# Optimization experiments

Measured on AMD Instinct MI355X. Metric: run time of the kernel, lower is better.

## Reference

```python
import jax, jax.numpy as jnp
import numpy as np

B, V, J, H, W = 32, 2, 17, 128, 128
TEMP = 0.05   # SoftArgmax2D softmax_temp
EPS = 1e-12


def _soft_argmax(hm):
    # hm: (B*V, J, H, W) -> homogeneous coords (B*V, 3, J), per-joint max value
    bv, j, h, w = hm.shape
    p = jax.nn.softmax(hm.reshape(bv, j, h * w) / TEMP, axis=-1).reshape(bv, j, h, w)
    xs = jnp.arange(w, dtype=hm.dtype)
    ys = jnp.arange(h, dtype=hm.dtype)
    x = jnp.einsum('bjhw,w->bj', p, xs)
    y = jnp.einsum('bjhw,h->bj', p, ys)
    coords = jnp.stack([x, y, jnp.ones_like(x)], axis=1)  # (bv, 3, j)
    maxv = hm.max(axis=(-2, -1))
    return coords, maxv


def _skew(t):
    # t: (..., 3) -> skew-symmetric (..., 3, 3), matches -t_mat^T + t_mat in source
    tx, ty, tz = t[..., 0], t[..., 1], t[..., 2]
    z = jnp.zeros_like(tx)
    return jnp.stack([jnp.stack([z, -tz, ty], -1),
                      jnp.stack([tz, z, -tx], -1),
                      jnp.stack([-ty, tx, z], -1)], -2)


def _forward(origin_hms, AP_K, AP_T, LAT_K, LAT_T):
    K = jnp.stack([AP_K, LAT_K], axis=1)              # (B,V,3,3)
    T = jnp.stack([AP_T, LAT_T], axis=1)              # (B,V,4,4)
    R = T[:, :, :3, :3]
    t_std = T[:, :, :3, 3]                            # (B,V,3) standard_cam_T

    # fundamental matrices for all ordered pairs: cam1 = view j, cam2 = view i
    r = jnp.einsum('bimk,bjnk->bijmn', R, R)          # R_i @ R_j^T
    t = t_std[:, :, None, :] - jnp.einsum('bijmn,bjn->bijm', r, t_std)
    M = jnp.einsum('bijmn,bijnk->bijmk', _skew(t), r)
    invK = jnp.linalg.inv(K)
    # F = invK_i^T @ [t]x @ r @ invK_j
    F = jnp.einsum('bipm,bijpq,bjql->bijml', invK, M, invK)  # (B,V,V,3,3)

    coords, maxv = _soft_argmax(origin_hms)           # (B*V,3,J), (B*V,J)
    inv_aff = jnp.diag(jnp.asarray([4.0, 4.0, 1.0], dtype=origin_hms.dtype))  # inverse of 0.25 scale
    img = jnp.einsum('mn,bvnj->bvmj', inv_aff, coords.reshape(B, V, 3, J))
    confi = maxv.reshape(B, V, J)

    # epipolar distances, fully vectorized over (b, i, j) pairs
    l = jnp.einsum('bijmn,bjnk->bijmk', F, img)       # epipolar lines in view i from joints of view j
    cv = img[:, :, None]                              # (B,V,1,3,J)
    num = jnp.sum(cv * l, axis=3) ** 2                # (B,V,V,J)
    lp = jnp.einsum('bijnm,bink->bijmk', F, img)      # F^T @ cv_joints
    div = l[..., 0, :] ** 2 + l[..., 1, :] ** 2 + lp[..., 0, :] ** 2 + lp[..., 1, :] ** 2
    dist_full = jnp.sqrt(num / (div + EPS))           # (B,V,V,J)

    others = np.asarray([[j for j in range(V) if j != i] for i in range(V)])  # (V,V-1)
    ii = np.repeat(np.arange(V)[:, None], V - 1, axis=1)
    distances = dist_full[:, ii, others]              # (B,V,V-1,J)

    # stand-in for ViewWeightNet: confidence minus mean epipolar error, softmax over views
    score = confi - distances.mean(axis=2)            # (B,V,J)
    vw = jax.nn.softmax(score, axis=1)                # (B,V,J)

    mv = jnp.where(maxv > 0.01, maxv, 1e6).reshape(B * V, J, 1, 1)
    hms_norm = origin_hms / mv
    hm4 = hms_norm.reshape(B, V, J, H, W)

    # cat order: self heatmap first, then other views (matches get_warp_weight / cat_hm layout)
    order = np.asarray([[i] + [j for j in range(V) if j != i] for i in range(V)])  # (V,V)
    cat_hm = hm4[:, order]                            # (B,V,V,J,H,W); identity-warp stand-in for CamFusionModule
    ww = vw[:, order]                                 # (B,V,V,J) warp weights
    fused_hm = jnp.sum(ww[..., None, None] * cat_hm, axis=2).reshape(B * V, J, H, W)

    coords2, _ = _soft_argmax(fused_hm)
    img2 = jnp.einsum('mn,bvnj->bvmj', inv_aff, coords2.reshape(B, V, 3, J))
    return img2[:, :, :2, :], fused_hm


def setup_inputs() -> dict:
    key = jax.random.key(0)
    k1, k2, k3, k4, k5 = jax.random.split(key, 5)
    hms = jax.random.uniform(k1, (B * V, J, H, W), dtype=jnp.float32)

    def make_K(k):
        f = 1000.0 + jax.random.normal(k, (B,)) * 10.0
        Km = jnp.zeros((B, 3, 3), dtype=jnp.float32)
        Km = Km.at[:, 0, 0].set(f).at[:, 1, 1].set(f)
        Km = Km.at[:, 0, 2].set(256.0).at[:, 1, 2].set(256.0).at[:, 2, 2].set(1.0)
        return Km

    def make_T(k):
        A = jax.random.normal(k, (B, 3, 3))
        Q, _ = jnp.linalg.qr(A)
        Q = Q * jnp.linalg.det(Q)[:, None, None]  # force det = +1 (proper rotation)
        t = jax.random.normal(jax.random.fold_in(k, 1), (B, 3, 1)) * 0.1 + jnp.asarray([0.0, 0.0, 5.0]).reshape(3, 1)
        bottom = jnp.tile(jnp.asarray([[[0.0, 0.0, 0.0, 1.0]]]), (B, 1, 1))
        return jnp.concatenate([jnp.concatenate([Q, t], axis=2), bottom], axis=1).astype(jnp.float32)

    return {"origin_hms": hms, "AP_K": make_K(k2), "AP_T": make_T(k3),
            "LAT_K": make_K(k4), "LAT_T": make_T(k5)}


def reference(origin_hms, AP_K, AP_T, LAT_K, LAT_T):
    return _forward(origin_hms, AP_K, AP_T, LAT_K, LAT_T)
```

## Files before the change

kernel.cpp:

```cpp
#include <hip/hip_runtime.h>
#include <math.h>

#define NB 32
#define NV 2
#define NJ 17
#define NH 128
#define NW 128
#define MAPN (NH * NW)
#define MAPN4 (MAPN / 4)
#define NMAPS (NB * NV * NJ)
#define NBJ (NB * NJ)
#define OUT0N (NB * NV * 2 * NJ)
#define INV_TEMP 20.0f
#define EPS_D 1e-12f

#define S_CHUNKS 4
#define S_F4 (MAPN4 / S_CHUNKS)
#define F_CHUNKS 8
#define F_F4 (MAPN4 / F_CHUNKS)

#define WS_STATS_B (NMAPS * S_CHUNKS * 16)
#define WS_W_B (NBJ * 2 * 4)
#define WS_F_B (NBJ * F_CHUNKS * 16)
#define WS_NEEDED (WS_STATS_B + WS_W_B + WS_F_B)

typedef float vfloat4 __attribute__((ext_vector_type(4)));

__device__ __forceinline__ float waveMax(float v) {
#pragma unroll
    for (int off = 32; off > 0; off >>= 1)
        v = fmaxf(v, __shfl_xor(v, off, 64));
    return v;
}
__device__ __forceinline__ float waveSum(float v) {
#pragma unroll
    for (int off = 32; off > 0; off >>= 1)
        v += __shfl_xor(v, off, 64);
    return v;
}

__device__ __forceinline__ void inv3(const float K[3][3], float o[3][3]) {
    const float a = K[0][0], b = K[0][1], c = K[0][2];
    const float d = K[1][0], e = K[1][1], f = K[1][2];
    const float g = K[2][0], h = K[2][1], i = K[2][2];
    const float A =  (e * i - f * h);
    const float Bv = -(d * i - f * g);
    const float C =  (d * h - e * g);
    const float det = a * A + b * Bv + c * C;
    const float id = 1.0f / det;
    o[0][0] = A * id;  o[0][1] = -(b * i - c * h) * id;  o[0][2] = (b * f - c * e) * id;
    o[1][0] = Bv * id; o[1][1] = (a * i - c * g) * id;   o[1][2] = -(a * f - c * d) * id;
    o[2][0] = C * id;  o[2][1] = -(a * h - b * g) * id;  o[2][2] = (a * e - b * d) * id;
}

__global__ __launch_bounds__(256, 4) void k_stats(const float* __restrict__ hms,
                                                  float* __restrict__ ws) {
    const int blk = blockIdx.x;
    const int mi = blk >> 2, c = blk & 3;
    const int tid = threadIdx.x, wid = tid >> 6, lane = tid & 63;
    const float4* A = (const float4*)hms + (size_t)mi * MAPN4 + (size_t)c * S_F4;

    float mx = -1e30f, s = 0.f, sx = 0.f, sy = 0.f;
#pragma unroll
    for (int k = 0; k < 4; ++k) {
        const int i4 = tid + k * 256;
        const float4 v = A[i4];
        const int e0 = (c * S_F4 + i4) * 4;
        const float hh = (float)(e0 >> 7);
        const float ww = (float)(e0 & 127);
        mx = fmaxf(mx, fmaxf(fmaxf(v.x, v.y), fmaxf(v.z, v.w)));
        const float ea = __expf((v.x - 1.0f) * INV_TEMP);
        const float eb = __expf((v.y - 1.0f) * INV_TEMP);
        const float ec = __expf((v.z - 1.0f) * INV_TEMP);
        const float ed = __expf((v.w - 1.0f) * INV_TEMP);
        const float se = (ea + eb) + (ec + ed);
        s += se; sy += se * hh;
        sx += ea * ww + eb * (ww + 1.f) + ec * (ww + 2.f) + ed * (ww + 3.f);
    }

    mx = waveMax(mx); s = waveSum(s); sx = waveSum(sx); sy = waveSum(sy);
    __shared__ float red[4][4];
    if (lane == 0) { red[0][wid] = mx; red[1][wid] = s; red[2][wid] = sx; red[3][wid] = sy; }
    __syncthreads();
    if (tid == 0) {
        float M = red[0][0], S = red[1][0], SX = red[2][0], SY = red[3][0];
#pragma unroll
        for (int w = 1; w < 4; ++w) {
            M = fmaxf(M, red[0][w]); S += red[1][w]; SX += red[2][w]; SY += red[3][w];
        }
        ((float4*)ws)[blk] = make_float4(M, S, SX, SY);
    }
}

__global__ void k_weights(const float* __restrict__ ws_stats,
                          const float* __restrict__ APK, const float* __restrict__ APT,
                          const float* __restrict__ LATK, const float* __restrict__ LATT,
                          float* __restrict__ wsw) {
    const int bj = blockIdx.x * 64 + threadIdx.x;
    if (bj >= NBJ) return;
    const int b = bj / NJ, j = bj % NJ;

    float conf[2], img[2][3];
    const float4* st = (const float4*)ws_stats;
#pragma unroll
    for (int v = 0; v < 2; ++v) {
        const int mi = (b * 2 + v) * NJ + j;
        float M = -1e30f, S = 0.f, SX = 0.f, SY = 0.f;
#pragma unroll
        for (int c = 0; c < S_CHUNKS; ++c) {
            const float4 p = st[mi * S_CHUNKS + c];
            M = fmaxf(M, p.x); S += p.y; SX += p.z; SY += p.w;
        }
        conf[v] = M;
        img[v][0] = 4.0f * (SX / S);
        img[v][1] = 4.0f * (SY / S);
        img[v][2] = 1.0f;
    }

    float F[2][3][3];
    {
        float Km[2][3][3], R[2][3][3], tr[2][3], iK[2][3][3];
        for (int r = 0; r < 3; ++r)
            for (int cc = 0; cc < 3; ++cc) {
                Km[0][r][cc] = APK[b * 9 + r * 3 + cc];
                Km[1][r][cc] = LATK[b * 9 + r * 3 + cc];
                R[0][r][cc] = APT[b * 16 + r * 4 + cc];
                R[1][r][cc] = LATT[b * 16 + r * 4 + cc];
            }
        for (int r = 0; r < 3; ++r) {
            tr[0][r] = APT[b * 16 + r * 4 + 3];
            tr[1][r] = LATT[b * 16 + r * 4 + 3];
        }
        inv3(Km[0], iK[0]);
        inv3(Km[1], iK[1]);

        for (int i = 0; i < 2; ++i) {
            const int jj = 1 - i;
            float r[3][3];
            for (int m = 0; m < 3; ++m)
                for (int n = 0; n < 3; ++n)
                    r[m][n] = R[i][m][0] * R[jj][n][0] + R[i][m][1] * R[jj][n][1] + R[i][m][2] * R[jj][n][2];
            float tv[3];
            for (int m = 0; m < 3; ++m)
                tv[m] = tr[i][m] - (r[m][0] * tr[jj][0] + r[m][1] * tr[jj][1] + r[m][2] * tr[jj][2]);
            const float S[3][3] = {{0.f, -tv[2], tv[1]}, {tv[2], 0.f, -tv[0]}, {-tv[1], tv[0], 0.f}};
            float M[3][3];
            for (int m = 0; m < 3; ++m)
                for (int n = 0; n < 3; ++n)
                    M[m][n] = S[m][0] * r[0][n] + S[m][1] * r[1][n] + S[m][2] * r[2][n];
            float tmp[3][3];
            for (int p = 0; p < 3; ++p)
                for (int l = 0; l < 3; ++l)
                    tmp[p][l] = M[p][0] * iK[jj][0][l] + M[p][1] * iK[jj][1][l] + M[p][2] * iK[jj][2][l];
            for (int m = 0; m < 3; ++m)
                for (int l = 0; l < 3; ++l)
                    F[i][m][l] = iK[i][0][m] * tmp[0][l] + iK[i][1][m] * tmp[1][l] + iK[i][2][m] * tmp[2][l];
        }
    }

    float score[2];
#pragma unroll
    for (int i = 0; i < 2; ++i) {
        const int jj = 1 - i;
        const float l0 = F[i][0][0] * img[jj][0] + F[i][0][1] * img[jj][1] + F[i][0][2] * img[jj][2];
        const float l1 = F[i][1][0] * img[jj][0] + F[i][1][1] * img[jj][1] + F[i][1][2] * img[jj][2];
        const float l2 = F[i][2][0] * img[jj][0] + F[i][2][1] * img[jj][1] + F[i][2][2] * img[jj][2];
        const float sdot = img[i][0] * l0 + img[i][1] * l1 + img[i][2] * l2;
        const float num = sdot * sdot;
        const float lp0 = F[i][0][0] * img[i][0] + F[i][1][0] * img[i][1] + F[i][2][0] * img[i][2];
        const float lp1 = F[i][0][1] * img[i][0] + F[i][1][1] * img[i][1] + F[i][2][1] * img[i][2];
        const float dv = l0 * l0 + l1 * l1 + lp0 * lp0 + lp1 * lp1;
        score[i] = conf[i] - sqrtf(num / (dv + EPS_D));
    }
    const float mS = fmaxf(score[0], score[1]);
    const float e0w = __expf(score[0] - mS), e1w = __expf(score[1] - mS);
    const float inv = 1.0f / (e0w + e1w);
    const float mv0 = conf[0] > 0.01f ? conf[0] : 1e6f;
    const float mv1 = conf[1] > 0.01f ? conf[1] : 1e6f;
    wsw[bj * 2 + 0] = (e0w * inv) / mv0;
    wsw[bj * 2 + 1] = (e1w * inv) / mv1;
}

__global__ __launch_bounds__(256, 4) void k_fuse(const float* __restrict__ hms,
                                                 const float* __restrict__ wsw,
                                                 float* __restrict__ out,
                                                 float* __restrict__ wsf) {
    const int blk = blockIdx.x;
    const int bj = blk >> 3, c = blk & 7;
    const int b = bj / NJ, j = bj % NJ;
    const int tid = threadIdx.x, wid = tid >> 6, lane = tid & 63;

    const float w0 = wsw[bj * 2 + 0];
    const float w1 = wsw[bj * 2 + 1];

    const size_t m0 = ((size_t)(b * 2 + 0) * NJ + j) * MAPN4;
    const size_t m1 = ((size_t)(b * 2 + 1) * NJ + j) * MAPN4;
    const float4* A  = (const float4*)hms + m0 + (size_t)c * F_F4;
    const float4* Bp = (const float4*)hms + m1 + (size_t)c * F_F4;
    float* outhm = out + OUT0N;
    vfloat4* O0 = reinterpret_cast<vfloat4*>(outhm) + m0 + (size_t)c * F_F4;
    vfloat4* O1 = reinterpret_cast<vfloat4*>(outhm) + m1 + (size_t)c * F_F4;

    float s = 0.f, sx = 0.f, sy = 0.f;
#pragma unroll
    for (int k = 0; k < 2; ++k) {
        const int i4 = tid + k * 256;
        const float4 a = A[i4];
        const float4 cc = Bp[i4];
        vfloat4 f;
        f.x = w0 * a.x + w1 * cc.x;
        f.y = w0 * a.y + w1 * cc.y;
        f.z = w0 * a.z + w1 * cc.z;
        f.w = w0 * a.w + w1 * cc.w;
        __builtin_nontemporal_store(f, &O0[i4]);
        __builtin_nontemporal_store(f, &O1[i4]);
        const int e0 = (c * F_F4 + i4) * 4;
        const float hh = (float)(e0 >> 7);
        const float ww = (float)(e0 & 127);
        const float ea = __expf((f.x - 1.0f) * INV_TEMP);
        const float eb = __expf((f.y - 1.0f) * INV_TEMP);
        const float ec = __expf((f.z - 1.0f) * INV_TEMP);
        const float ed = __expf((f.w - 1.0f) * INV_TEMP);
        const float se = (ea + eb) + (ec + ed);
        s += se; sy += se * hh;
        sx += ea * ww + eb * (ww + 1.f) + ec * (ww + 2.f) + ed * (ww + 3.f);
    }

    s = waveSum(s); sx = waveSum(sx); sy = waveSum(sy);
    __shared__ float red[3][4];
    if (lane == 0) { red[0][wid] = s; red[1][wid] = sx; red[2][wid] = sy; }
    __syncthreads();
    if (tid == 0) {
        float S = red[0][0], SX = red[1][0], SY = red[2][0];
#pragma unroll
        for (int w = 1; w < 4; ++w) { S += red[0][w]; SX += red[1][w]; SY += red[2][w]; }
        ((float4*)wsf)[blk] = make_float4(S, SX, SY, 0.f);
    }
}

__global__ void k_out(const float* __restrict__ wsf, float* __restrict__ out) {
    const int bj = blockIdx.x * 64 + threadIdx.x;
    if (bj >= NBJ) return;
    const int b = bj / NJ, j = bj % NJ;
    const float4* p = (const float4*)wsf + bj * F_CHUNKS;
    float S = 0.f, SX = 0.f, SY = 0.f;
#pragma unroll
    for (int c = 0; c < F_CHUNKS; ++c) {
        const float4 q = p[c];
        S += q.x; SX += q.y; SY += q.z;
    }
    const float x4 = 4.0f * (SX / S);
    const float y4 = 4.0f * (SY / S);
    out[((b * 2 + 0) * 2 + 0) * NJ + j] = x4;
    out[((b * 2 + 0) * 2 + 1) * NJ + j] = y4;
    out[((b * 2 + 1) * 2 + 0) * NJ + j] = x4;
    out[((b * 2 + 1) * 2 + 1) * NJ + j] = y4;
}

__global__ __launch_bounds__(512, 2) void k_one(const float* __restrict__ hms,
                                                const float* __restrict__ APK,
                                                const float* __restrict__ APT,
                                                const float* __restrict__ LATK,
                                                const float* __restrict__ LATT,
                                                float* __restrict__ out) {
    const int blk = blockIdx.x;
    const int b = blk / NJ, j = blk % NJ;
    const int tid = threadIdx.x;
    const int wid = tid >> 6, lane = tid & 63;

    float F[2][3][3];
    {
        float Km[2][3][3], R[2][3][3], tr[2][3], iK[2][3][3];
        for (int r = 0; r < 3; ++r)
            for (int c = 0; c < 3; ++c) {
                Km[0][r][c] = APK[b * 9 + r * 3 + c];
                Km[1][r][c] = LATK[b * 9 + r * 3 + c];
                R[0][r][c] = APT[b * 16 + r * 4 + c];
                R[1][r][c] = LATT[b * 16 + r * 4 + c];
            }
        for (int r = 0; r < 3; ++r) {
            tr[0][r] = APT[b * 16 + r * 4 + 3];
            tr[1][r] = LATT[b * 16 + r * 4 + 3];
        }
        inv3(Km[0], iK[0]);
        inv3(Km[1], iK[1]);

        for (int i = 0; i < 2; ++i) {
            const int jj = 1 - i;
            float r[3][3];
            for (int m = 0; m < 3; ++m)
                for (int n = 0; n < 3; ++n)
                    r[m][n] = R[i][m][0] * R[jj][n][0] + R[i][m][1] * R[jj][n][1] + R[i][m][2] * R[jj][n][2];
            float tv[3];
            for (int m = 0; m < 3; ++m)
                tv[m] = tr[i][m] - (r[m][0] * tr[jj][0] + r[m][1] * tr[jj][1] + r[m][2] * tr[jj][2]);
            const float S[3][3] = {{0.f, -tv[2], tv[1]}, {tv[2], 0.f, -tv[0]}, {-tv[1], tv[0], 0.f}};
            float M[3][3];
            for (int m = 0; m < 3; ++m)
                for (int n = 0; n < 3; ++n)
                    M[m][n] = S[m][0] * r[0][n] + S[m][1] * r[1][n] + S[m][2] * r[2][n];
            float tmp[3][3];
            for (int p = 0; p < 3; ++p)
                for (int l = 0; l < 3; ++l)
                    tmp[p][l] = M[p][0] * iK[jj][0][l] + M[p][1] * iK[jj][1][l] + M[p][2] * iK[jj][2][l];
            for (int m = 0; m < 3; ++m)
                for (int l = 0; l < 3; ++l)
                    F[i][m][l] = iK[i][0][m] * tmp[0][l] + iK[i][1][m] * tmp[1][l] + iK[i][2][m] * tmp[2][l];
        }
    }

    const int idx0 = (b * 2 + 0) * NJ + j;
    const int idx1 = (b * 2 + 1) * NJ + j;
    const size_t m0 = (size_t)idx0 * MAPN4;
    const size_t m1 = (size_t)idx1 * MAPN4;
    const float4* A  = (const float4*)hms + m0;
    const float4* Bp = (const float4*)hms + m1;

    float4 va[8];
    float mx0 = -1e30f, s0 = 0.f, sx0 = 0.f, sy0 = 0.f;
    float mx1 = -1e30f, s1 = 0.f, sx1 = 0.f, sy1 = 0.f;
#pragma unroll
    for (int u = 0; u < 8; ++u) {
        const int i4 = tid + u * 512;
        const float4 v = A[i4];
        const float4 w = Bp[i4];
        va[u] = v;
        const int e0 = i4 * 4;
        const float hh = (float)(e0 >> 7);
        const float ww = (float)(e0 & 127);
        {
            mx0 = fmaxf(mx0, fmaxf(fmaxf(v.x, v.y), fmaxf(v.z, v.w)));
            const float ea = __expf((v.x - 1.0f) * INV_TEMP);
            const float eb = __expf((v.y - 1.0f) * INV_TEMP);
            const float ec = __expf((v.z - 1.0f) * INV_TEMP);
            const float ed = __expf((v.w - 1.0f) * INV_TEMP);
            const float se = (ea + eb) + (ec + ed);
            s0 += se; sy0 += se * hh;
            sx0 += ea * ww + eb * (ww + 1.f) + ec * (ww + 2.f) + ed * (ww + 3.f);
        }
        {
            mx1 = fmaxf(mx1, fmaxf(fmaxf(w.x, w.y), fmaxf(w.z, w.w)));
            const float ea = __expf((w.x - 1.0f) * INV_TEMP);
            const float eb = __expf((w.y - 1.0f) * INV_TEMP);
            const float ec = __expf((w.z - 1.0f) * INV_TEMP);
            const float ed = __expf((w.w - 1.0f) * INV_TEMP);
            const float se = (ea + eb) + (ec + ed);
            s1 += se; sy1 += se * hh;
            sx1 += ea * ww + eb * (ww + 1.f) + ec * (ww + 2.f) + ed * (ww + 3.f);
        }
    }

    __shared__ float red[8][8];
    mx0 = waveMax(mx0); mx1 = waveMax(mx1);
    s0 = waveSum(s0); sx0 = waveSum(sx0); sy0 = waveSum(sy0);
    s1 = waveSum(s1); sx1 = waveSum(sx1); sy1 = waveSum(sy1);
    if (lane == 0) {
        red[0][wid] = mx0; red[1][wid] = s0; red[2][wid] = sx0; red[3][wid] = sy0;
        red[4][wid] = mx1; red[5][wid] = s1; red[6][wid] = sx1; red[7][wid] = sy1;
    }
    __syncthreads();
    float M0 = red[0][0], S0 = red[1][0], SX0 = red[2][0], SY0 = red[3][0];
    float M1 = red[4][0], S1 = red[5][0], SX1 = red[6][0], SY1 = red[7][0];
#pragma unroll
    for (int w = 1; w < 8; ++w) {
        M0 = fmaxf(M0, red[0][w]); S0 += red[1][w]; SX0 += red[2][w]; SY0 += red[3][w];
        M1 = fmaxf(M1, red[4][w]); S1 += red[5][w]; SX1 += red[6][w]; SY1 += red[7][w];
    }

    float w0, w1;
    {
        const float conf[2] = {M0, M1};
        float img[2][3];
        img[0][0] = 4.0f * (SX0 / S0); img[0][1] = 4.0f * (SY0 / S0); img[0][2] = 1.0f;
        img[1][0] = 4.0f * (SX1 / S1); img[1][1] = 4.0f * (SY1 / S1); img[1][2] = 1.0f;

        float score[2];
        for (int i = 0; i < 2; ++i) {
            const int jj = 1 - i;
            const float l0 = F[i][0][0] * img[jj][0] + F[i][0][1] * img[jj][1] + F[i][0][2] * img[jj][2];
            const float l1 = F[i][1][0] * img[jj][0] + F[i][1][1] * img[jj][1] + F[i][1][2] * img[jj][2];
            const float l2 = F[i][2][0] * img[jj][0] + F[i][2][1] * img[jj][1] + F[i][2][2] * img[jj][2];
            const float sdot = img[i][0] * l0 + img[i][1] * l1 + img[i][2] * l2;
            const float num = sdot * sdot;
            const float lp0 = F[i][0][0] * img[i][0] + F[i][1][0] * img[i][1] + F[i][2][0] * img[i][2];
            const float lp1 = F[i][0][1] * img[i][0] + F[i][1][1] * img[i][1] + F[i][2][1] * img[i][2];
            const float dv = l0 * l0 + l1 * l1 + lp0 * lp0 + lp1 * lp1;
            score[i] = conf[i] - sqrtf(num / (dv + EPS_D));
        }
        const float mS = fmaxf(score[0], score[1]);
        const float e0w = __expf(score[0] - mS), e1w = __expf(score[1] - mS);
        const float inv = 1.0f / (e0w + e1w);
        const float mv0 = conf[0] > 0.01f ? conf[0] : 1e6f;
        const float mv1 = conf[1] > 0.01f ? conf[1] : 1e6f;
        w0 = (e0w * inv) / mv0;
        w1 = (e1w * inv) / mv1;
    }

    float* outhm = out + OUT0N;
    vfloat4* O0 = reinterpret_cast<vfloat4*>(outhm) + m0;
    vfloat4* O1 = reinterpret_cast<vfloat4*>(outhm) + m1;

    float s = 0.f, sx = 0.f, sy = 0.f;
#pragma unroll
    for (int u = 0; u < 8; ++u) {
        const int i4 = tid + u * 512;
        const float4 a = va[u];
        const float4 c = Bp[i4];
        vfloat4 f;
        f.x = w0 * a.x + w1 * c.x;
        f.y = w0 * a.y + w1 * c.y;
        f.z = w0 * a.z + w1 * c.z;
        f.w = w0 * a.w + w1 * c.w;
        __builtin_nontemporal_store(f, &O0[i4]);
        __builtin_nontemporal_store(f, &O1[i4]);
        const int e0 = i4 * 4;
        const float hh = (float)(e0 >> 7);
        const float ww = (float)(e0 & 127);
        const float ea = __expf((f.x - 1.0f) * INV_TEMP);
        const float eb = __expf((f.y - 1.0f) * INV_TEMP);
        const float ec = __expf((f.z - 1.0f) * INV_TEMP);
        const float ed = __expf((f.w - 1.0f) * INV_TEMP);
        const float se = (ea + eb) + (ec + ed);
        s += se; sy += se * hh;
        sx += ea * ww + eb * (ww + 1.f) + ec * (ww + 2.f) + ed * (ww + 3.f);
    }

    __syncthreads();
    s = waveSum(s); sx = waveSum(sx); sy = waveSum(sy);
    if (lane == 0) { red[0][wid] = s; red[1][wid] = sx; red[2][wid] = sy; }
    __syncthreads();
    if (tid == 0) {
        float S = red[0][0], SX = red[1][0], SY = red[2][0];
#pragma unroll
        for (int w = 1; w < 8; ++w) { S += red[0][w]; SX += red[1][w]; SY += red[2][w]; }
        const float x4 = 4.0f * (SX / S);
        const float y4 = 4.0f * (SY / S);
        out[((b * 2 + 0) * 2 + 0) * NJ + j] = x4;
        out[((b * 2 + 0) * 2 + 1) * NJ + j] = y4;
        out[((b * 2 + 1) * 2 + 0) * NJ + j] = x4;
        out[((b * 2 + 1) * 2 + 1) * NJ + j] = y4;
    }
}

extern "C" void kernel_launch(void* const* d_in, const int* in_sizes, int n_in,
                              void* d_out, int out_size, void* d_ws, size_t ws_size,
                              hipStream_t stream) {
    const float* hms  = (const float*)d_in[0];
    const float* APK  = (const float*)d_in[1];
    const float* APT  = (const float*)d_in[2];
    const float* LATK = (const float*)d_in[3];
    const float* LATT = (const float*)d_in[4];
    float* out = (float*)d_out;

    if (d_ws != nullptr && ws_size >= (size_t)WS_NEEDED) {
        float* ws_stats = (float*)d_ws;
        float* ws_w = ws_stats + NMAPS * S_CHUNKS * 4;
        float* ws_f = ws_w + NBJ * 2;
        k_stats<<<NMAPS * S_CHUNKS, 256, 0, stream>>>(hms, ws_stats);
        k_weights<<<(NBJ + 63) / 64, 64, 0, stream>>>(ws_stats, APK, APT, LATK, LATT, ws_w);
        k_fuse<<<NBJ * F_CHUNKS, 256, 0, stream>>>(hms, ws_w, out, ws_f);
        k_out<<<(NBJ + 63) / 64, 64, 0, stream>>>(ws_f, out);
    } else {
        k_one<<<NBJ, 512, 0, stream>>>(hms, APK, APT, LATK, LATT, out);
    }
}
```

Baseline: 141.9 us.

## Fold weight and output kernels into stats and fuse kernels

Reduces the four-kernel pipeline to two. The fundamental matrices are computed once per batch inside the stats kernel, and the per-joint view weights are recomputed inside each fuse block. The final coordinate reduction is handled by the last-arriving block through an atomic counter with threadfences. In the fuse kernel the heatmap loads are issued before the weight computation so their latency overlaps it, and k_stats launch bounds rise to 8 blocks per CU. This removes two small-kernel launches and their serialization gaps, at the cost of redundant per-block weight arithmetic and atomic synchronization.

```diff
diff --git a/kernel.cpp b/kernel.cpp
--- a/kernel.cpp
+++ b/kernel.cpp
@@ -19,10 +19,11 @@
 #define F_CHUNKS 8
 #define F_F4 (MAPN4 / F_CHUNKS)
 
-#define WS_STATS_B (NMAPS * S_CHUNKS * 16)
-#define WS_W_B (NBJ * 2 * 4)
-#define WS_F_B (NBJ * F_CHUNKS * 16)
-#define WS_NEEDED (WS_STATS_B + WS_W_B + WS_F_B)
+#define WS_STATS_F (NMAPS * S_CHUNKS * 4)
+#define WS_F_F (32 * 20)
+#define WS_CNT_F (NBJ)
+#define WS_FP_F (NBJ * F_CHUNKS * 4)
+#define WS_NEEDED ((WS_STATS_F + WS_F_F + WS_CNT_F + WS_FP_F) * 4)
 
 typedef float vfloat4 __attribute__((ext_vector_type(4)));
 
@@ -53,11 +54,71 @@
     o[2][0] = C * id;  o[2][1] = -(a * h - b * g) * id;  o[2][2] = (a * e - b * d) * id;
 }
 
-__global__ __launch_bounds__(256, 4) void k_stats(const float* __restrict__ hms,
-                                                  float* __restrict__ ws) {
+__device__ void computeF(int b, const float* APK, const float* APT,
+                         const float* LATK, const float* LATT, float F[2][3][3]) {
+    float Km[2][3][3], R[2][3][3], tr[2][3], iK[2][3][3];
+    for (int r = 0; r < 3; ++r)
+        for (int cc = 0; cc < 3; ++cc) {
+            Km[0][r][cc] = APK[b * 9 + r * 3 + cc];
+            Km[1][r][cc] = LATK[b * 9 + r * 3 + cc];
+            R[0][r][cc] = APT[b * 16 + r * 4 + cc];
+            R[1][r][cc] = LATT[b * 16 + r * 4 + cc];
+        }
+    for (int r = 0; r < 3; ++r) {
+        tr[0][r] = APT[b * 16 + r * 4 + 3];
+        tr[1][r] = LATT[b * 16 + r * 4 + 3];
+    }
+    inv3(Km[0], iK[0]);
+    inv3(Km[1], iK[1]);
+
+    for (int i = 0; i < 2; ++i) {
+        const int jj = 1 - i;
+        float r[3][3];
+        for (int m = 0; m < 3; ++m)
+            for (int n = 0; n < 3; ++n)
+                r[m][n] = R[i][m][0] * R[jj][n][0] + R[i][m][1] * R[jj][n][1] + R[i][m][2] * R[jj][n][2];
+        float tv[3];
+        for (int m = 0; m < 3; ++m)
+            tv[m] = tr[i][m] - (r[m][0] * tr[jj][0] + r[m][1] * tr[jj][1] + r[m][2] * tr[jj][2]);
+        const float S[3][3] = {{0.f, -tv[2], tv[1]}, {tv[2], 0.f, -tv[0]}, {-tv[1], tv[0], 0.f}};
+        float M[3][3];
+        for (int m = 0; m < 3; ++m)
+            for (int n = 0; n < 3; ++n)
+                M[m][n] = S[m][0] * r[0][n] + S[m][1] * r[1][n] + S[m][2] * r[2][n];
+        float tmp[3][3];
+        for (int p = 0; p < 3; ++p)
+            for (int l = 0; l < 3; ++l)
+                tmp[p][l] = M[p][0] * iK[jj][0][l] + M[p][1] * iK[jj][1][l] + M[p][2] * iK[jj][2][l];
+        for (int m = 0; m < 3; ++m)
+            for (int l = 0; l < 3; ++l)
+                F[i][m][l] = iK[i][0][m] * tmp[0][l] + iK[i][1][m] * tmp[1][l] + iK[i][2][m] * tmp[2][l];
+    }
+}
+
+__global__ __launch_bounds__(256, 8) void k_stats(const float* __restrict__ hms,
+                                                  const float* __restrict__ APK,
+                                                  const float* __restrict__ APT,
+                                                  const float* __restrict__ LATK,
+                                                  const float* __restrict__ LATT,
+                                                  float* __restrict__ ws_stats,
+                                                  float* __restrict__ wsF,
+                                                  unsigned int* __restrict__ cnt) {
     const int blk = blockIdx.x;
     const int mi = blk >> 2, c = blk & 3;
     const int tid = threadIdx.x, wid = tid >> 6, lane = tid & 63;
+
+    if (tid == 64 && blk < NBJ) cnt[blk] = 0u;
+    if (tid == 128 && blk < NB) {
+        float F[2][3][3];
+        computeF(blk, APK, APT, LATK, LATT, F);
+        float* d = wsF + blk * 20;
+#pragma unroll
+        for (int i = 0; i < 2; ++i)
+            for (int m = 0; m < 3; ++m)
+                for (int l = 0; l < 3; ++l)
+                    d[i * 9 + m * 3 + l] = F[i][m][l];
+    }
+
     const float4* A = (const float4*)hms + (size_t)mi * MAPN4 + (size_t)c * S_F4;
 
     float mx = -1e30f, s = 0.f, sx = 0.f, sy = 0.f;
@@ -88,115 +149,85 @@
         for (int w = 1; w < 4; ++w) {
             M = fmaxf(M, red[0][w]); S += red[1][w]; SX += red[2][w]; SY += red[3][w];
         }
-        ((float4*)ws)[blk] = make_float4(M, S, SX, SY);
-    }
-}
-
-__global__ void k_weights(const float* __restrict__ ws_stats,
-                          const float* __restrict__ APK, const float* __restrict__ APT,
-                          const float* __restrict__ LATK, const float* __restrict__ LATT,
-                          float* __restrict__ wsw) {
-    const int bj = blockIdx.x * 64 + threadIdx.x;
-    if (bj >= NBJ) return;
-    const int b = bj / NJ, j = bj % NJ;
-
-    float conf[2], img[2][3];
-    const float4* st = (const float4*)ws_stats;
-#pragma unroll
-    for (int v = 0; v < 2; ++v) {
-        const int mi = (b * 2 + v) * NJ + j;
-        float M = -1e30f, S = 0.f, SX = 0.f, SY = 0.f;
-#pragma unroll
-        for (int c = 0; c < S_CHUNKS; ++c) {
-            const float4 p = st[mi * S_CHUNKS + c];
-            M = fmaxf(M, p.x); S += p.y; SX += p.z; SY += p.w;
-        }
-        conf[v] = M;
-        img[v][0] = 4.0f * (SX / S);
-        img[v][1] = 4.0f * (SY / S);
-        img[v][2] = 1.0f;
-    }
-
-    float F[2][3][3];
-    {
-        float Km[2][3][3], R[2][3][3], tr[2][3], iK[2][3][3];
-        for (int r = 0; r < 3; ++r)
-            for (int cc = 0; cc < 3; ++cc) {
-                Km[0][r][cc] = APK[b * 9 + r * 3 + cc];
-                Km[1][r][cc] = LATK[b * 9 + r * 3 + cc];
-                R[0][r][cc] = APT[b * 16 + r * 4 + cc];
-                R[1][r][cc] = LATT[b * 16 + r * 4 + cc];
-            }
-        for (int r = 0; r < 3; ++r) {
-            tr[0][r] = APT[b * 16 + r * 4 + 3];
-            tr[1][r] = LATT[b * 16 + r * 4 + 3];
-        }
-        inv3(Km[0], iK[0]);
-        inv3(Km[1], iK[1]);
-
-        for (int i = 0; i < 2; ++i) {
-            const int jj = 1 - i;
-            float r[3][3];
-            for (int m = 0; m < 3; ++m)
-                for (int n = 0; n < 3; ++n)
-                    r[m][n] = R[i][m][0] * R[jj][n][0] + R[i][m][1] * R[jj][n][1] + R[i][m][2] * R[jj][n][2];
-            float tv[3];
-            for (int m = 0; m < 3; ++m)
-                tv[m] = tr[i][m] - (r[m][0] * tr[jj][0] + r[m][1] * tr[jj][1] + r[m][2] * tr[jj][2]);
-            const float S[3][3] = {{0.f, -tv[2], tv[1]}, {tv[2], 0.f, -tv[0]}, {-tv[1], tv[0], 0.f}};
-            float M[3][3];
-            for (int m = 0; m < 3; ++m)
-                for (int n = 0; n < 3; ++n)
-                    M[m][n] = S[m][0] * r[0][n] + S[m][1] * r[1][n] + S[m][2] * r[2][n];
-            float tmp[3][3];
-            for (int p = 0; p < 3; ++p)
-                for (int l = 0; l < 3; ++l)
-                    tmp[p][l] = M[p][0] * iK[jj][0][l] + M[p][1] * iK[jj][1][l] + M[p][2] * iK[jj][2][l];
-            for (int m = 0; m < 3; ++m)
-                for (int l = 0; l < 3; ++l)
-                    F[i][m][l] = iK[i][0][m] * tmp[0][l] + iK[i][1][m] * tmp[1][l] + iK[i][2][m] * tmp[2][l];
-        }
-    }
-
-    float score[2];
-#pragma unroll
-    for (int i = 0; i < 2; ++i) {
-        const int jj = 1 - i;
-        const float l0 = F[i][0][0] * img[jj][0] + F[i][0][1] * img[jj][1] + F[i][0][2] * img[jj][2];
-        const float l1 = F[i][1][0] * img[jj][0] + F[i][1][1] * img[jj][1] + F[i][1][2] * img[jj][2];
-        const float l2 = F[i][2][0] * img[jj][0] + F[i][2][1] * img[jj][1] + F[i][2][2] * img[jj][2];
-        const float sdot = img[i][0] * l0 + img[i][1] * l1 + img[i][2] * l2;
-        const float num = sdot * sdot;
-        const float lp0 = F[i][0][0] * img[i][0] + F[i][1][0] * img[i][1] + F[i][2][0] * img[i][2];
-        const float lp1 = F[i][0][1] * img[i][0] + F[i][1][1] * img[i][1] + F[i][2][1] * img[i][2];
-        const float dv = l0 * l0 + l1 * l1 + lp0 * lp0 + lp1 * lp1;
-        score[i] = conf[i] - sqrtf(num / (dv + EPS_D));
-    }
-    const float mS = fmaxf(score[0], score[1]);
-    const float e0w = __expf(score[0] - mS), e1w = __expf(score[1] - mS);
-    const float inv = 1.0f / (e0w + e1w);
-    const float mv0 = conf[0] > 0.01f ? conf[0] : 1e6f;
-    const float mv1 = conf[1] > 0.01f ? conf[1] : 1e6f;
-    wsw[bj * 2 + 0] = (e0w * inv) / mv0;
-    wsw[bj * 2 + 1] = (e1w * inv) / mv1;
+        ((float4*)ws_stats)[blk] = make_float4(M, S, SX, SY);
+    }
 }
 
 __global__ __launch_bounds__(256, 4) void k_fuse(const float* __restrict__ hms,
-                                                 const float* __restrict__ wsw,
-                                                 float* __restrict__ out,
-                                                 float* __restrict__ wsf) {
+                                                 const float* __restrict__ ws_stats,
+                                                 const float* __restrict__ wsF,
+                                                 unsigned int* __restrict__ cnt,
+                                                 float* __restrict__ ws_fp,
+                                                 float* __restrict__ out) {
     const int blk = blockIdx.x;
     const int bj = blk >> 3, c = blk & 7;
     const int b = bj / NJ, j = bj % NJ;
     const int tid = threadIdx.x, wid = tid >> 6, lane = tid & 63;
 
-    const float w0 = wsw[bj * 2 + 0];
-    const float w1 = wsw[bj * 2 + 1];
-
     const size_t m0 = ((size_t)(b * 2 + 0) * NJ + j) * MAPN4;
     const size_t m1 = ((size_t)(b * 2 + 1) * NJ + j) * MAPN4;
     const float4* A  = (const float4*)hms + m0 + (size_t)c * F_F4;
     const float4* Bp = (const float4*)hms + m1 + (size_t)c * F_F4;
+
+    float4 av[2], bv[2];
+#pragma unroll
+    for (int k = 0; k < 2; ++k) {
+        const int i4 = tid + k * 256;
+        av[k] = A[i4];
+        bv[k] = Bp[i4];
+    }
+
+    float w0, w1;
+    {
+        const int mi0 = (b * 2 + 0) * NJ + j;
+        const int mi1 = (b * 2 + 1) * NJ + j;
+        const float4* st = (const float4*)ws_stats;
+        float conf[2], img[2][3];
+#pragma unroll
+        for (int v = 0; v < 2; ++v) {
+            const int mi = v ? mi1 : mi0;
+            float M = -1e30f, S = 0.f, SX = 0.f, SY = 0.f;
+#pragma unroll
+            for (int cc = 0; cc < S_CHUNKS; ++cc) {
+                const float4 p = st[mi * S_CHUNKS + cc];
+                M = fmaxf(M, p.x); S += p.y; SX += p.z; SY += p.w;
+            }
+            conf[v] = M;
+            img[v][0] = 4.0f * (SX / S);
+            img[v][1] = 4.0f * (SY / S);
+            img[v][2] = 1.0f;
+        }
+        const float* Fb = wsF + b * 20;
+        float F[2][3][3];
+#pragma unroll
+        for (int i = 0; i < 2; ++i)
+            for (int m = 0; m < 3; ++m)
+                for (int l = 0; l < 3; ++l)
+                    F[i][m][l] = Fb[i * 9 + m * 3 + l];
+
+        float score[2];
+#pragma unroll
+        for (int i = 0; i < 2; ++i) {
+            const int jj = 1 - i;
+            const float l0 = F[i][0][0] * img[jj][0] + F[i][0][1] * img[jj][1] + F[i][0][2] * img[jj][2];
+            const float l1 = F[i][1][0] * img[jj][0] + F[i][1][1] * img[jj][1] + F[i][1][2] * img[jj][2];
+            const float l2 = F[i][2][0] * img[jj][0] + F[i][2][1] * img[jj][1] + F[i][2][2] * img[jj][2];
+            const float sdot = img[i][0] * l0 + img[i][1] * l1 + img[i][2] * l2;
+            const float num = sdot * sdot;
+            const float lp0 = F[i][0][0] * img[i][0] + F[i][1][0] * img[i][1] + F[i][2][0] * img[i][2];
+            const float lp1 = F[i][0][1] * img[i][0] + F[i][1][1] * img[i][1] + F[i][2][1] * img[i][2];
+            const float dv = l0 * l0 + l1 * l1 + lp0 * lp0 + lp1 * lp1;
+            score[i] = conf[i] - sqrtf(num / (dv + EPS_D));
+        }
+        const float mS = fmaxf(score[0], score[1]);
+        const float e0w = __expf(score[0] - mS), e1w = __expf(score[1] - mS);
+        const float inv = 1.0f / (e0w + e1w);
+        const float mv0 = conf[0] > 0.01f ? conf[0] : 1e6f;
+        const float mv1 = conf[1] > 0.01f ? conf[1] : 1e6f;
+        w0 = (e0w * inv) / mv0;
+        w1 = (e1w * inv) / mv1;
+    }
+
     float* outhm = out + OUT0N;
     vfloat4* O0 = reinterpret_cast<vfloat4*>(outhm) + m0 + (size_t)c * F_F4;
     vfloat4* O1 = reinterpret_cast<vfloat4*>(outhm) + m1 + (size_t)c * F_F4;
@@ -205,8 +236,8 @@
 #pragma unroll
     for (int k = 0; k < 2; ++k) {
         const int i4 = tid + k * 256;
-        const float4 a = A[i4];
-        const float4 cc = Bp[i4];
+        const float4 a = av[k];
+        const float4 cc = bv[k];
         vfloat4 f;
         f.x = w0 * a.x + w1 * cc.x;
         f.y = w0 * a.y + w1 * cc.y;
@@ -234,27 +265,27 @@
         float S = red[0][0], SX = red[1][0], SY = red[2][0];
 #pragma unroll
         for (int w = 1; w < 4; ++w) { S += red[0][w]; SX += red[1][w]; SY += red[2][w]; }
-        ((float4*)wsf)[blk] = make_float4(S, SX, SY, 0.f);
-    }
-}
-
-__global__ void k_out(const float* __restrict__ wsf, float* __restrict__ out) {
-    const int bj = blockIdx.x * 64 + threadIdx.x;
-    if (bj >= NBJ) return;
-    const int b = bj / NJ, j = bj % NJ;
-    const float4* p = (const float4*)wsf + bj * F_CHUNKS;
-    float S = 0.f, SX = 0.f, SY = 0.f;
-#pragma unroll
-    for (int c = 0; c < F_CHUNKS; ++c) {
-        const float4 q = p[c];
-        S += q.x; SX += q.y; SY += q.z;
-    }
-    const float x4 = 4.0f * (SX / S);
-    const float y4 = 4.0f * (SY / S);
-    out[((b * 2 + 0) * 2 + 0) * NJ + j] = x4;
-    out[((b * 2 + 0) * 2 + 1) * NJ + j] = y4;
-    out[((b * 2 + 1) * 2 + 0) * NJ + j] = x4;
-    out[((b * 2 + 1) * 2 + 1) * NJ + j] = y4;
+        ((float4*)ws_fp)[blk] = make_float4(S, SX, SY, 0.f);
+        __threadfence();
+        const unsigned int old = atomicAdd(&cnt[bj], 1u);
+        if (old == F_CHUNKS - 1) {
+            __threadfence();
+            const volatile float* vp = (const volatile float*)ws_fp + (size_t)bj * (F_CHUNKS * 4);
+            float TS = 0.f, TX = 0.f, TY = 0.f;
+#pragma unroll
+            for (int q = 0; q < F_CHUNKS; ++q) {
+                TS += vp[q * 4 + 0];
+                TX += vp[q * 4 + 1];
+                TY += vp[q * 4 + 2];
+            }
+            const float x4 = 4.0f * (TX / TS);
+            const float y4 = 4.0f * (TY / TS);
+            out[((b * 2 + 0) * 2 + 0) * NJ + j] = x4;
+            out[((b * 2 + 0) * 2 + 1) * NJ + j] = y4;
+            out[((b * 2 + 1) * 2 + 0) * NJ + j] = x4;
+            out[((b * 2 + 1) * 2 + 1) * NJ + j] = y4;
+        }
+    }
 }
 
 __global__ __launch_bounds__(512, 2) void k_one(const float* __restrict__ hms,
@@ -269,45 +300,7 @@
     const int wid = tid >> 6, lane = tid & 63;
 
     float F[2][3][3];
-    {
-        float Km[2][3][3], R[2][3][3], tr[2][3], iK[2][3][3];
-        for (int r = 0; r < 3; ++r)
-            for (int c = 0; c < 3; ++c) {
-                Km[0][r][c] = APK[b * 9 + r * 3 + c];
-                Km[1][r][c] = LATK[b * 9 + r * 3 + c];
-                R[0][r][c] = APT[b * 16 + r * 4 + c];
-                R[1][r][c] = LATT[b * 16 + r * 4 + c];
-            }
-        for (int r = 0; r < 3; ++r) {
-            tr[0][r] = APT[b * 16 + r * 4 + 3];
-            tr[1][r] = LATT[b * 16 + r * 4 + 3];
-        }
-        inv3(Km[0], iK[0]);
-        inv3(Km[1], iK[1]);
-
-        for (int i = 0; i < 2; ++i) {
-            const int jj = 1 - i;
-            float r[3][3];
-            for (int m = 0; m < 3; ++m)
-                for (int n = 0; n < 3; ++n)
-                    r[m][n] = R[i][m][0] * R[jj][n][0] + R[i][m][1] * R[jj][n][1] + R[i][m][2] * R[jj][n][2];
-            float tv[3];
-            for (int m = 0; m < 3; ++m)
-                tv[m] = tr[i][m] - (r[m][0] * tr[jj][0] + r[m][1] * tr[jj][1] + r[m][2] * tr[jj][2]);
-            const float S[3][3] = {{0.f, -tv[2], tv[1]}, {tv[2], 0.f, -tv[0]}, {-tv[1], tv[0], 0.f}};
-            float M[3][3];
-            for (int m = 0; m < 3; ++m)
-                for (int n = 0; n < 3; ++n)
-                    M[m][n] = S[m][0] * r[0][n] + S[m][1] * r[1][n] + S[m][2] * r[2][n];
-            float tmp[3][3];
-            for (int p = 0; p < 3; ++p)
-                for (int l = 0; l < 3; ++l)
-                    tmp[p][l] = M[p][0] * iK[jj][0][l] + M[p][1] * iK[jj][1][l] + M[p][2] * iK[jj][2][l];
-            for (int m = 0; m < 3; ++m)
-                for (int l = 0; l < 3; ++l)
-                    F[i][m][l] = iK[i][0][m] * tmp[0][l] + iK[i][1][m] * tmp[1][l] + iK[i][2][m] * tmp[2][l];
-        }
-    }
+    computeF(b, APK, APT, LATK, LATT, F);
 
     const int idx0 = (b * 2 + 0) * NJ + j;
     const int idx1 = (b * 2 + 1) * NJ + j;
@@ -454,12 +447,12 @@
 
     if (d_ws != nullptr && ws_size >= (size_t)WS_NEEDED) {
         float* ws_stats = (float*)d_ws;
-        float* ws_w = ws_stats + NMAPS * S_CHUNKS * 4;
-        float* ws_f = ws_w + NBJ * 2;
-        k_stats<<<NMAPS * S_CHUNKS, 256, 0, stream>>>(hms, ws_stats);
-        k_weights<<<(NBJ + 63) / 64, 64, 0, stream>>>(ws_stats, APK, APT, LATK, LATT, ws_w);
-        k_fuse<<<NBJ * F_CHUNKS, 256, 0, stream>>>(hms, ws_w, out, ws_f);
-        k_out<<<(NBJ + 63) / 64, 64, 0, stream>>>(ws_f, out);
+        float* wsF = ws_stats + WS_STATS_F;
+        unsigned int* cnt = (unsigned int*)(wsF + WS_F_F);
+        float* ws_fp = (float*)(cnt + WS_CNT_F);
+        k_stats<<<NMAPS * S_CHUNKS, 256, 0, stream>>>(hms, APK, APT, LATK, LATT,
+                                                      ws_stats, wsF, cnt);
+        k_fuse<<<NBJ * F_CHUNKS, 256, 0, stream>>>(hms, ws_stats, wsF, cnt, ws_fp, out);
     } else {
         k_one<<<NBJ, 512, 0, stream>>>(hms, APK, APT, LATK, LATT, out);
     }
```

Measured after the change: 339.9 us. +139.6%, slower.
